# Performance work log

Measured on AMD Instinct MI355X. Metric: run time of the kernel, lower is better.

Reference implementation:

```python
import jax, jax.numpy as jnp
import numpy as np

RES = 200        # self.res, hard-coded in the module
MODES_OUT = 16
MODES_IN = 32
T_SEQ = 10
D_MODEL = 256
BATCH = 16


def setup_inputs() -> dict:
    key = jax.random.key(0)
    k1, k2, k3 = jax.random.split(key, 3)
    v = jax.random.normal(k1, (BATCH, T_SEQ, D_MODEL, 2, MODES_IN), dtype=jnp.float32)
    scale = 1.0 / (MODES_IN * MODES_OUT)
    # weights1 = scale * rand(T,1,1,mo,mi) cfloat; singleton dims broadcast -> store as [T,mo,mi]
    w_real = scale * jax.random.uniform(k2, (T_SEQ, MODES_OUT, MODES_IN), dtype=jnp.float32)
    w_imag = scale * jax.random.uniform(k3, (T_SEQ, MODES_OUT, MODES_IN), dtype=jnp.float32)
    return {"v": v, "w_real": w_real, "w_imag": w_imag}


def reference(v, w_real, w_imag):
    # v: [B,T,H,2,mi] -> complex x_ft = r + i*1j
    r = v[:, :, :, 0, :]  # [B,T,H,mi]
    i = v[:, :, :, 1, :]
    # einsum 'bthix,thiox->bthox' with h=i=1 in weights == broadcast complex multiply
    wr = w_real[None, :, None, :, :]  # [1,T,1,mo,mi]
    wi = w_imag[None, :, None, :, :]
    rr = r[:, :, :, None, :]          # [B,T,H,1,mi]
    ii = i[:, :, :, None, :]
    re = rr * wr - ii * wi            # [B,T,H,mo,mi] = Re(out_ft)
    im = rr * wi + ii * wr            # Im(out_ft)
    amp = jax.nn.relu(jnp.sqrt(re * re + im * im))  # relu(|out_ft|)
    ph = jnp.arctan2(im, re)                          # angle(out_ft)
    # cosine reconstruction grid: theta[o,x] = 2*pi*f_o*x, f from fftfreq(res, d=1/(res-1))
    x_res = jnp.linspace(0.0, 1.0, RES).astype(jnp.float32)
    dx = x_res[1] - x_res[0]
    freqs = jnp.fft.fftfreq(RES, d=dx)[:MODES_OUT].astype(jnp.float32)  # [mo]
    theta = (2.0 * jnp.pi) * freqs[:, None] * x_res[None, :]            # [mo,res]
    # sum over mi of amp*cos(theta + ph) = cos(theta)*sum(amp*cos ph) - sin(theta)*sum(amp*sin ph)
    # (exact trig identity; avoids materializing the 6-D [B,T,H,mo,mi,res] tensor)
    C = jnp.sum(amp * jnp.cos(ph), axis=-1)  # [B,T,H,mo]
    S = jnp.sum(amp * jnp.sin(ph), axis=-1)  # [B,T,H,mo]
    out = (jnp.einsum('btho,ox->btxh', C, jnp.cos(theta))
           - jnp.einsum('btho,ox->btxh', S, jnp.sin(theta)))  # [B,T,res,H]
    return out
```

## Files before the change

### kernel.cpp

```cpp
#include <hip/hip_runtime.h>

#define B_   16
#define T_   10
#define D_   256
#define MI_  32
#define MO_  16
#define RES_ 200
#define TWO_PI 6.28318530717958647692f

#define HSLICE 32
#define NHS    (D_ / HSLICE)
#define VPAD   68
#define BT_STRIDE (2 * MO_ * D_)

using f32x4 = __attribute__((ext_vector_type(4))) float;
using v2f   = __attribute__((ext_vector_type(2))) float;

__global__ __launch_bounds__(256) void spectral_cs(
    const float* __restrict__ v,
    const float* __restrict__ w_real,
    const float* __restrict__ w_imag,
    float* __restrict__ ws)
{
    const int blk = blockIdx.x;
    const int bt  = blk >> 3;
    const int hs  = blk & 7;
    const int t   = bt % T_;

    __shared__ float s_v[HSLICE * VPAD];

    {
        const float4* gv = reinterpret_cast<const float4*>(
            v + ((size_t)bt * D_ + hs * HSLICE) * (2 * MI_));
        #pragma unroll
        for (int j = 0; j < 2; ++j) {
            const int f = threadIdx.x + 256 * j;
            const int h = f >> 4;
            const int m = (f & 15) * 4;
            *reinterpret_cast<float4*>(&s_v[h * VPAD + m]) = gv[f];
        }
    }
    __syncthreads();

    const int og  = threadIdx.x >> 5;
    const int h_l = threadIdx.x & 31;
    const int o0  = og * 2;
    const int h_g = hs * HSLICE + h_l;

    float rr[MI_], ii[MI_];
    #pragma unroll
    for (int j = 0; j < 8; ++j) {
        float4 q = *reinterpret_cast<const float4*>(&s_v[h_l * VPAD + 4 * j]);
        rr[4*j+0]=q.x; rr[4*j+1]=q.y; rr[4*j+2]=q.z; rr[4*j+3]=q.w;
    }
    #pragma unroll
    for (int j = 0; j < 8; ++j) {
        float4 q = *reinterpret_cast<const float4*>(&s_v[h_l * VPAD + 32 + 4 * j]);
        ii[4*j+0]=q.x; ii[4*j+1]=q.y; ii[4*j+2]=q.z; ii[4*j+3]=q.w;
    }

    const float* wrt = w_real + ((size_t)t * MO_ + o0) * MI_;
    const float* wit = w_imag + ((size_t)t * MO_ + o0) * MI_;

    float* wsb = ws + (size_t)bt * BT_STRIDE;
    #pragma unroll
    for (int ol = 0; ol < 2; ++ol) {
        const float4* wa = reinterpret_cast<const float4*>(wrt + ol * MI_);
        const float4* wb = reinterpret_cast<const float4*>(wit + ol * MI_);
        float c = 0.f, s = 0.f;
        #pragma unroll
        for (int mq = 0; mq < 8; ++mq) {
            float4 a4 = wa[mq];
            float4 b4 = wb[mq];
            c = fmaf(rr[4*mq+0], a4.x, c); c = fmaf(-ii[4*mq+0], b4.x, c);
            s = fmaf(rr[4*mq+0], b4.x, s); s = fmaf( ii[4*mq+0], a4.x, s);
            c = fmaf(rr[4*mq+1], a4.y, c); c = fmaf(-ii[4*mq+1], b4.y, c);
            s = fmaf(rr[4*mq+1], b4.y, s); s = fmaf( ii[4*mq+1], a4.y, s);
            c = fmaf(rr[4*mq+2], a4.z, c); c = fmaf(-ii[4*mq+2], b4.z, c);
            s = fmaf(rr[4*mq+2], b4.z, s); s = fmaf( ii[4*mq+2], a4.z, s);
            c = fmaf(rr[4*mq+3], a4.w, c); c = fmaf(-ii[4*mq+3], b4.w, c);
            s = fmaf(rr[4*mq+3], b4.w, s); s = fmaf( ii[4*mq+3], a4.w, s);
        }
        const int o = o0 + ol;
        v2f p; p.x = c; p.y = s;
        *reinterpret_cast<v2f*>(&wsb[2 * (o * D_ + h_g)]) = p;
    }
}

__global__ __launch_bounds__(256) void spectral_ift(
    const float* __restrict__ ws,
    float* __restrict__ out)
{
    const int blk  = blockIdx.x;
    const int bt   = blk >> 2;
    const int qb   = blk & 3;
    const int wave = threadIdx.x >> 6;
    const int lane = threadIdx.x & 63;
    const int g    = qb * 4 + wave;
    const int h0   = lane * 4;

    const float* wsb = ws + (size_t)bt * BT_STRIDE;
    v2f CS0[MO_], CS1[MO_], CS2[MO_], CS3[MO_];
    #pragma unroll
    for (int o = 0; o < MO_; ++o) {
        float4 q0 = *reinterpret_cast<const float4*>(&wsb[2 * (o * D_ + h0)]);
        float4 q1 = *reinterpret_cast<const float4*>(&wsb[2 * (o * D_ + h0) + 4]);
        CS0[o].x = q0.x; CS0[o].y = q0.y;
        CS1[o].x = q0.z; CS1[o].y = q0.w;
        CS2[o].x = q1.x; CS2[o].y = q1.y;
        CS3[o].x = q1.z; CS3[o].y = q1.w;
    }

    float* ob = out + (size_t)bt * RES_ * D_;

    #pragma unroll
    for (int k = 0; k < 7; ++k) {
        const int s = g + 16 * k;
        if (s <= 100) {
            const float phi = (float)s * (TWO_PI / (float)RES_);
            float s1, c1;
            __sincosf(phi, &s1, &c1);

            v2f ab0 = {0.f, 0.f}, ab1 = {0.f, 0.f};
            v2f ab2 = {0.f, 0.f}, ab3 = {0.f, 0.f};
            v2f cs;  cs.x = 1.f; cs.y = 0.f;
            #pragma unroll
            for (int o = 0; o < MO_; ++o) {
                ab0 = __builtin_elementwise_fma(CS0[o], cs, ab0);
                ab1 = __builtin_elementwise_fma(CS1[o], cs, ab1);
                ab2 = __builtin_elementwise_fma(CS2[o], cs, ab2);
                ab3 = __builtin_elementwise_fma(CS3[o], cs, ab3);
                const float nc = fmaf(cs.x, c1, -(cs.y * s1));
                const float ns = fmaf(cs.y, c1,  (cs.x * s1));
                cs.x = nc; cs.y = ns;
            }

            const int mr = (s == 0) ? 0 : (RES_ - s);
            f32x4 lo, hi;
            lo.x = ab0.x - ab0.y; hi.x = ab0.x + ab0.y;
            lo.y = ab1.x - ab1.y; hi.y = ab1.x + ab1.y;
            lo.z = ab2.x - ab2.y; hi.z = ab2.x + ab2.y;
            lo.w = ab3.x - ab3.y; hi.w = ab3.x + ab3.y;
            __builtin_nontemporal_store(
                lo, reinterpret_cast<f32x4*>(&ob[(size_t)s  * D_ + h0]));
            __builtin_nontemporal_store(
                hi, reinterpret_cast<f32x4*>(&ob[(size_t)mr * D_ + h0]));
        }
    }
}

extern "C" void kernel_launch(void* const* d_in, const int* in_sizes, int n_in,
                              void* d_out, int out_size, void* d_ws, size_t ws_size,
                              hipStream_t stream) {
    const float* v  = (const float*)d_in[0];
    const float* wr = (const float*)d_in[1];
    const float* wi = (const float*)d_in[2];
    float* out = (float*)d_out;
    float* ws  = (float*)d_ws;

    spectral_cs <<<B_ * T_ * NHS, 256, 0, stream>>>(v, wr, wi, ws);
    spectral_ift<<<B_ * T_ * 4,   256, 0, stream>>>(ws, out);
}
```

Measured before the change: 24.99 us.

## Fuse C/S projection and cosine reconstruction into one kernel via shared memory

Merges the two kernels into a single 512-thread kernel per (b,t, half of H). C/S coefficients now stay in LDS instead of taking a round trip through the global workspace, and one launch replaces two. In exchange the grid shrinks to 320 blocks, each with larger LDS use and more work per block, which may lower occupancy and parallelism on the device.

```diff
diff --git a/kernel.cpp b/kernel.cpp
--- a/kernel.cpp
+++ b/kernel.cpp
@@ -8,33 +8,33 @@
 #define RES_ 200
 #define TWO_PI 6.28318530717958647692f
 
-#define HSLICE 32
-#define NHS    (D_ / HSLICE)
-#define VPAD   68
-#define BT_STRIDE (2 * MO_ * D_)
+#define HH    128
+#define VPAD  68
+#define CSN   (MO_ * HH)
 
 using f32x4 = __attribute__((ext_vector_type(4))) float;
 using v2f   = __attribute__((ext_vector_type(2))) float;
 
-__global__ __launch_bounds__(256) void spectral_cs(
+__global__ __launch_bounds__(512) void spectral_fused1(
     const float* __restrict__ v,
     const float* __restrict__ w_real,
     const float* __restrict__ w_imag,
-    float* __restrict__ ws)
+    float* __restrict__ out)
 {
     const int blk = blockIdx.x;
-    const int bt  = blk >> 3;
-    const int hs  = blk & 7;
+    const int bt  = blk >> 1;
+    const int hh  = blk & 1;
     const int t   = bt % T_;
 
-    __shared__ float s_v[HSLICE * VPAD];
+    __shared__ float s_v[HH * VPAD];
+    __shared__ float s_cs[2 * CSN];
 
     {
         const float4* gv = reinterpret_cast<const float4*>(
-            v + ((size_t)bt * D_ + hs * HSLICE) * (2 * MI_));
+            v + ((size_t)bt * D_ + hh * HH) * (2 * MI_));
         #pragma unroll
-        for (int j = 0; j < 2; ++j) {
-            const int f = threadIdx.x + 256 * j;
+        for (int j = 0; j < 4; ++j) {
+            const int f = threadIdx.x + 512 * j;
             const int h = f >> 4;
             const int m = (f & 15) * 4;
             *reinterpret_cast<float4*>(&s_v[h * VPAD + m]) = gv[f];
@@ -42,109 +42,105 @@
     }
     __syncthreads();
 
-    const int og  = threadIdx.x >> 5;
-    const int h_l = threadIdx.x & 31;
-    const int o0  = og * 2;
-    const int h_g = hs * HSLICE + h_l;
+    {
+        const int og  = threadIdx.x & 3;
+        const int h_l = threadIdx.x >> 2;
 
-    float rr[MI_], ii[MI_];
-    #pragma unroll
-    for (int j = 0; j < 8; ++j) {
-        float4 q = *reinterpret_cast<const float4*>(&s_v[h_l * VPAD + 4 * j]);
-        rr[4*j+0]=q.x; rr[4*j+1]=q.y; rr[4*j+2]=q.z; rr[4*j+3]=q.w;
+        float rr[MI_], ii[MI_];
+        #pragma unroll
+        for (int j = 0; j < 8; ++j) {
+            float4 q = *reinterpret_cast<const float4*>(&s_v[h_l * VPAD + 4 * j]);
+            rr[4*j+0]=q.x; rr[4*j+1]=q.y; rr[4*j+2]=q.z; rr[4*j+3]=q.w;
+        }
+        #pragma unroll
+        for (int j = 0; j < 8; ++j) {
+            float4 q = *reinterpret_cast<const float4*>(&s_v[h_l * VPAD + 32 + 4 * j]);
+            ii[4*j+0]=q.x; ii[4*j+1]=q.y; ii[4*j+2]=q.z; ii[4*j+3]=q.w;
+        }
+
+        const int o0 = og * 4;
+        const float* wrt = w_real + ((size_t)t * MO_ + o0) * MI_;
+        const float* wit = w_imag + ((size_t)t * MO_ + o0) * MI_;
+
+        #pragma unroll
+        for (int ol = 0; ol < 4; ++ol) {
+            const float4* wa = reinterpret_cast<const float4*>(wrt + ol * MI_);
+            const float4* wb = reinterpret_cast<const float4*>(wit + ol * MI_);
+            float c = 0.f, s = 0.f;
+            #pragma unroll
+            for (int mq = 0; mq < 8; ++mq) {
+                float4 a4 = wa[mq];
+                float4 b4 = wb[mq];
+                c = fmaf(rr[4*mq+0], a4.x, c); c = fmaf(-ii[4*mq+0], b4.x, c);
+                s = fmaf(rr[4*mq+0], b4.x, s); s = fmaf( ii[4*mq+0], a4.x, s);
+                c = fmaf(rr[4*mq+1], a4.y, c); c = fmaf(-ii[4*mq+1], b4.y, c);
+                s = fmaf(rr[4*mq+1], b4.y, s); s = fmaf( ii[4*mq+1], a4.y, s);
+                c = fmaf(rr[4*mq+2], a4.z, c); c = fmaf(-ii[4*mq+2], b4.z, c);
+                s = fmaf(rr[4*mq+2], b4.z, s); s = fmaf( ii[4*mq+2], a4.z, s);
+                c = fmaf(rr[4*mq+3], a4.w, c); c = fmaf(-ii[4*mq+3], b4.w, c);
+                s = fmaf(rr[4*mq+3], b4.w, s); s = fmaf( ii[4*mq+3], a4.w, s);
+            }
+            const int o = o0 + ol;
+            v2f p; p.x = c; p.y = s;
+            *reinterpret_cast<v2f*>(&s_cs[2 * (o * HH + h_l)]) = p;
+        }
     }
-    #pragma unroll
-    for (int j = 0; j < 8; ++j) {
-        float4 q = *reinterpret_cast<const float4*>(&s_v[h_l * VPAD + 32 + 4 * j]);
-        ii[4*j+0]=q.x; ii[4*j+1]=q.y; ii[4*j+2]=q.z; ii[4*j+3]=q.w;
-    }
+    __syncthreads();
 
-    const float* wrt = w_real + ((size_t)t * MO_ + o0) * MI_;
-    const float* wit = w_imag + ((size_t)t * MO_ + o0) * MI_;
+    {
+        const int wave   = threadIdx.x >> 6;
+        const int lane   = threadIdx.x & 63;
+        const int sub    = lane >> 5;
+        const int li     = lane & 31;
+        const int stream = wave * 2 + sub;
+        const int h0     = li * 4;
 
-    float* wsb = ws + (size_t)bt * BT_STRIDE;
-    #pragma unroll
-    for (int ol = 0; ol < 2; ++ol) {
-        const float4* wa = reinterpret_cast<const float4*>(wrt + ol * MI_);
-        const float4* wb = reinterpret_cast<const float4*>(wit + ol * MI_);
-        float c = 0.f, s = 0.f;
+        v2f CS0[MO_], CS1[MO_], CS2[MO_], CS3[MO_];
         #pragma unroll
-        for (int mq = 0; mq < 8; ++mq) {
-            float4 a4 = wa[mq];
-            float4 b4 = wb[mq];
-            c = fmaf(rr[4*mq+0], a4.x, c); c = fmaf(-ii[4*mq+0], b4.x, c);
-            s = fmaf(rr[4*mq+0], b4.x, s); s = fmaf( ii[4*mq+0], a4.x, s);
-            c = fmaf(rr[4*mq+1], a4.y, c); c = fmaf(-ii[4*mq+1], b4.y, c);
-            s = fmaf(rr[4*mq+1], b4.y, s); s = fmaf( ii[4*mq+1], a4.y, s);
-            c = fmaf(rr[4*mq+2], a4.z, c); c = fmaf(-ii[4*mq+2], b4.z, c);
-            s = fmaf(rr[4*mq+2], b4.z, s); s = fmaf( ii[4*mq+2], a4.z, s);
-            c = fmaf(rr[4*mq+3], a4.w, c); c = fmaf(-ii[4*mq+3], b4.w, c);
-            s = fmaf(rr[4*mq+3], b4.w, s); s = fmaf( ii[4*mq+3], a4.w, s);
+        for (int o = 0; o < MO_; ++o) {
+            float4 q0 = *reinterpret_cast<const float4*>(&s_cs[2 * (o * HH + h0)]);
+            float4 q1 = *reinterpret_cast<const float4*>(&s_cs[2 * (o * HH + h0) + 4]);
+            CS0[o].x = q0.x; CS0[o].y = q0.y;
+            CS1[o].x = q0.z; CS1[o].y = q0.w;
+            CS2[o].x = q1.x; CS2[o].y = q1.y;
+            CS3[o].x = q1.z; CS3[o].y = q1.w;
         }
-        const int o = o0 + ol;
-        v2f p; p.x = c; p.y = s;
-        *reinterpret_cast<v2f*>(&wsb[2 * (o * D_ + h_g)]) = p;
-    }
-}
 
-__global__ __launch_bounds__(256) void spectral_ift(
-    const float* __restrict__ ws,
-    float* __restrict__ out)
-{
-    const int blk  = blockIdx.x;
-    const int bt   = blk >> 2;
-    const int qb   = blk & 3;
-    const int wave = threadIdx.x >> 6;
-    const int lane = threadIdx.x & 63;
-    const int g    = qb * 4 + wave;
-    const int h0   = lane * 4;
+        float* ob = out + (size_t)bt * RES_ * D_ + hh * HH + h0;
 
-    const float* wsb = ws + (size_t)bt * BT_STRIDE;
-    v2f CS0[MO_], CS1[MO_], CS2[MO_], CS3[MO_];
-    #pragma unroll
-    for (int o = 0; o < MO_; ++o) {
-        float4 q0 = *reinterpret_cast<const float4*>(&wsb[2 * (o * D_ + h0)]);
-        float4 q1 = *reinterpret_cast<const float4*>(&wsb[2 * (o * D_ + h0) + 4]);
-        CS0[o].x = q0.x; CS0[o].y = q0.y;
-        CS1[o].x = q0.z; CS1[o].y = q0.w;
-        CS2[o].x = q1.x; CS2[o].y = q1.y;
-        CS3[o].x = q1.z; CS3[o].y = q1.w;
-    }
+        #pragma unroll
+        for (int k = 0; k < 7; ++k) {
+            const int s = stream + 16 * k;
+            if (s <= 100) {
+                const float phi = (float)s * (TWO_PI / (float)RES_);
+                float s1, c1;
+                __sincosf(phi, &s1, &c1);
 
-    float* ob = out + (size_t)bt * RES_ * D_;
+                v2f ab0 = {0.f, 0.f}, ab1 = {0.f, 0.f};
+                v2f ab2 = {0.f, 0.f}, ab3 = {0.f, 0.f};
+                v2f cs;  cs.x = 1.f; cs.y = 0.f;
+                #pragma unroll
+                for (int o = 0; o < MO_; ++o) {
+                    ab0 = __builtin_elementwise_fma(CS0[o], cs, ab0);
+                    ab1 = __builtin_elementwise_fma(CS1[o], cs, ab1);
+                    ab2 = __builtin_elementwise_fma(CS2[o], cs, ab2);
+                    ab3 = __builtin_elementwise_fma(CS3[o], cs, ab3);
+                    const float nc = fmaf(cs.x, c1, -(cs.y * s1));
+                    const float ns = fmaf(cs.y, c1,  (cs.x * s1));
+                    cs.x = nc; cs.y = ns;
+                }
 
-    #pragma unroll
-    for (int k = 0; k < 7; ++k) {
-        const int s = g + 16 * k;
-        if (s <= 100) {
-            const float phi = (float)s * (TWO_PI / (float)RES_);
-            float s1, c1;
-            __sincosf(phi, &s1, &c1);
-
-            v2f ab0 = {0.f, 0.f}, ab1 = {0.f, 0.f};
-            v2f ab2 = {0.f, 0.f}, ab3 = {0.f, 0.f};
-            v2f cs;  cs.x = 1.f; cs.y = 0.f;
-            #pragma unroll
-            for (int o = 0; o < MO_; ++o) {
-                ab0 = __builtin_elementwise_fma(CS0[o], cs, ab0);
-                ab1 = __builtin_elementwise_fma(CS1[o], cs, ab1);
-                ab2 = __builtin_elementwise_fma(CS2[o], cs, ab2);
-                ab3 = __builtin_elementwise_fma(CS3[o], cs, ab3);
-                const float nc = fmaf(cs.x, c1, -(cs.y * s1));
-                const float ns = fmaf(cs.y, c1,  (cs.x * s1));
-                cs.x = nc; cs.y = ns;
+                const int mr = (s == 0) ? 0 : (RES_ - s);
+                f32x4 lo, hi;
+                lo.x = ab0.x - ab0.y; hi.x = ab0.x + ab0.y;
+                lo.y = ab1.x - ab1.y; hi.y = ab1.x + ab1.y;
+                lo.z = ab2.x - ab2.y; hi.z = ab2.x + ab2.y;
+                lo.w = ab3.x - ab3.y; hi.w = ab3.x + ab3.y;
+                __builtin_nontemporal_store(
+                    lo, reinterpret_cast<f32x4*>(&ob[(size_t)s  * D_]));
+                __builtin_nontemporal_store(
+                    hi, reinterpret_cast<f32x4*>(&ob[(size_t)mr * D_]));
             }
-
-            const int mr = (s == 0) ? 0 : (RES_ - s);
-            f32x4 lo, hi;
-            lo.x = ab0.x - ab0.y; hi.x = ab0.x + ab0.y;
-            lo.y = ab1.x - ab1.y; hi.y = ab1.x + ab1.y;
-            lo.z = ab2.x - ab2.y; hi.z = ab2.x + ab2.y;
-            lo.w = ab3.x - ab3.y; hi.w = ab3.x + ab3.y;
-            __builtin_nontemporal_store(
-                lo, reinterpret_cast<f32x4*>(&ob[(size_t)s  * D_ + h0]));
-            __builtin_nontemporal_store(
-                hi, reinterpret_cast<f32x4*>(&ob[(size_t)mr * D_ + h0]));
         }
     }
 }
@@ -156,8 +152,5 @@
     const float* wr = (const float*)d_in[1];
     const float* wi = (const float*)d_in[2];
     float* out = (float*)d_out;
-    float* ws  = (float*)d_ws;
-
-    spectral_cs <<<B_ * T_ * NHS, 256, 0, stream>>>(v, wr, wi, ws);
-    spectral_ift<<<B_ * T_ * 4,   256, 0, stream>>>(ws, out);
+    spectral_fused1<<<B_ * T_ * 2, 512, 0, stream>>>(v, wr, wi, out);
 }
```

Result: slower. 42.84 us (+71.4%).
